# Kernel tuning notes

Hardware: AMD Instinct MI355X
Metric: run time of the kernel (lower is better)

The kernel has to match this reference:

```python
import jax, jax.numpy as jnp
import numpy as np

EPS = 1e-5      # BatchNorm eps (eval mode, running stats at init: mean=0, var=1)
SLOPE = 0.2     # LeakyReLU negative slope


def _knn_idx(x, k):
    # x: (B, N, D) -> (B, N, k) indices of k nearest neighbors (squared L2, feature space)
    sq = jnp.sum(x * x, axis=-1)                              # (B, N)
    dist = sq[:, :, None] + sq[:, None, :] - 2.0 * jnp.einsum('bnd,bmd->bnm', x, x)
    return jax.lax.top_k(-dist, k)[1]                         # nearest = largest of -dist


def _bn_lrelu(y, gamma, beta):
    # eval BatchNorm with running_mean=0, running_var=1, then LeakyReLU(0.2)
    y = y * (gamma / jnp.sqrt(1.0 + EPS)) + beta
    return jnp.where(y >= 0, y, SLOPE * y)


def _edge_conv(x, W, gamma, beta, k):
    # x: (B, N, D); W: (C_out, 2D). Returns (B, N, C_out) after max over k neighbors.
    idx = _knn_idx(x, k)                                      # (B, N, k)
    nb = jax.vmap(lambda xt, i: xt[i])(x, idx)                # (B, N, k, D) neighbor gather
    ctr = jnp.broadcast_to(x[:, :, None, :], nb.shape)
    feat = jnp.concatenate([nb - ctr, ctr], axis=-1)          # (B, N, k, 2D)
    y = jnp.einsum('bnkd,od->bnko', feat, W)                  # 1x1 conv (no bias)
    y = _bn_lrelu(y, gamma, beta)
    return jnp.max(y, axis=2)                                 # max-pool over neighbors


def setup_inputs() -> dict:
    key = jax.random.key(0)
    ks = jax.random.split(key, 16)
    B, N, k, out_dim = 8, 4096, 20, 512
    x = jax.random.normal(ks[0], (B, 3, N), dtype=jnp.float32)
    dims = [(64, 6), (64, 128), (128, 128), (256, 256), (out_dim, 512)]
    inp = {'x': x, 'k': k}
    for i, (co, ci) in enumerate(dims, start=1):
        inp[f'W{i}'] = jax.random.normal(ks[3 * i - 2], (co, ci), dtype=jnp.float32) * (1.0 / np.sqrt(ci))
        inp[f'g{i}'] = jax.random.uniform(ks[3 * i - 1], (co,), dtype=jnp.float32, minval=0.5, maxval=1.5)
        inp[f'b{i}'] = 0.1 * jax.random.normal(ks[3 * i], (co,), dtype=jnp.float32)
    return inp


def reference(x, W1, g1, b1, W2, g2, b2, W3, g3, b3, W4, g4, b4, W5, g5, b5, k):
    xt = jnp.transpose(x, (0, 2, 1))                          # (B, N, 3)
    x1 = _edge_conv(xt, W1, g1, b1, k)                        # (B, N, 64)
    x2 = _edge_conv(x1, W2, g2, b2, k)                        # (B, N, 64)
    x3 = _edge_conv(x2, W3, g3, b3, k)                        # (B, N, 128)
    x4 = _edge_conv(x3, W4, g4, b4, k)                        # (B, N, 256)
    h = jnp.concatenate([x1, x2, x3, x4], axis=-1)            # (B, N, 512)
    y = _bn_lrelu(jnp.einsum('bnd,od->bno', h, W5), g5, b5)   # (B, N, out_dim)
    return jnp.concatenate([jnp.max(y, axis=1), jnp.mean(y, axis=1)], axis=-1)  # (B, 2*out_dim)
```

## Files before the change

kernel.cpp:

```cpp
#include <hip/hip_runtime.h>
#include <math.h>

#define BATCH 8
#define N_PTS 4096
#define KNN 20
#define EPS_BN 1e-5f
#define SLOPE 0.2f
#define M_ROWS (BATCH * N_PTS)

typedef __attribute__((ext_vector_type(8))) short short8;
typedef __attribute__((ext_vector_type(4))) float float4v;
typedef __attribute__((ext_vector_type(16))) float float16v;

__device__ __forceinline__ unsigned short f2bf(float f) {
    unsigned u = __float_as_uint(f);
    unsigned r = (u + 0x7FFFu + ((u >> 16) & 1u)) >> 16;
    return (unsigned short)r;
}
__device__ __forceinline__ float bf2f(unsigned short h) {
    return __uint_as_float((unsigned)h << 16);
}

__global__ void convert_x1(const float* __restrict__ x,
                           unsigned short* __restrict__ xh, unsigned short* __restrict__ xl,
                           float* __restrict__ sq) {
    int i = blockIdx.x * blockDim.x + threadIdx.x;
    if (i >= M_ROWS) return;
    int b = i / N_PTS, n = i % N_PTS;
    float v[3], s = 0.f;
    #pragma unroll
    for (int d = 0; d < 3; ++d) {
        v[d] = x[((size_t)b * 3 + d) * N_PTS + n];
        s += v[d] * v[d];
    }
    sq[i] = s;
    #pragma unroll
    for (int d = 0; d < 32; ++d) {
        float f = (d < 3) ? v[d] : 0.f;
        unsigned short h = f2bf(f);
        xh[(size_t)i * 32 + d] = h;
        xl[(size_t)i * 32 + d] = f2bf(f - bf2f(h));
    }
}

__global__ void sqnorm_hl(const unsigned short* __restrict__ hh,
                          const unsigned short* __restrict__ hl,
                          int D, float* __restrict__ sq) {
    int w = threadIdx.x >> 6, lane = threadIdx.x & 63;
    int row = blockIdx.x * 4 + w;
    if (row >= M_ROWS) return;
    const unsigned short* ph = hh + (size_t)row * 512;
    const unsigned short* pl = hl + (size_t)row * 512;
    float s = 0.f;
    for (int d = lane; d < D; d += 64) {
        float v = bf2f(ph[d]) + bf2f(pl[d]);
        s += v * v;
    }
    #pragma unroll
    for (int off = 32; off > 0; off >>= 1) s += __shfl_down(s, off, 64);
    if (lane == 0) sq[row] = s;
}

__global__ void repack_edge_split(const float* __restrict__ W, int Co, int D, int KP,
                                  unsigned short* __restrict__ Wh, unsigned short* __restrict__ Wl) {
    int i = blockIdx.x * blockDim.x + threadIdx.x;
    int tot = 2 * Co * KP;
    if (i >= tot) return;
    int r = i / KP, d = i % KP;
    float v = 0.f;
    if (d < D) v = (r < Co) ? W[(size_t)r * 2 * D + d] : W[(size_t)(r - Co) * 2 * D + D + d];
    unsigned short h = f2bf(v);
    Wh[i] = h; Wl[i] = f2bf(v - bf2f(h));
}

__global__ void repack_w5_split(const float* __restrict__ W,
                                unsigned short* __restrict__ Wh, unsigned short* __restrict__ Wl) {
    int i = blockIdx.x * blockDim.x + threadIdx.x;
    if (i >= 512 * 512) return;
    float v = W[i];
    unsigned short h = f2bf(v);
    Wh[i] = h; Wl[i] = f2bf(v - bf2f(h));
}

template<int DPAD>
__global__ void
__launch_bounds__(256)
__attribute__((amdgpu_waves_per_eu(2, 2)))
knn_mfma(const unsigned short* __restrict__ Xh,
         const unsigned short* __restrict__ Xl,
         int strideX,
         const float* __restrict__ sq, int* __restrict__ idxout) {
    constexpr int KS = DPAD / 16;
    constexpr size_t MAIN  = (size_t)4096 * 4 + (size_t)256 * 17 * 4;
    constexpr size_t MERGE = (size_t)64 * 4 * KNN * 8;
    constexpr size_t POOL  = MAIN > MERGE ? MAIN : MERGE;
    __shared__ __align__(16) char smem[POOL];
    float* sqs = (float*)smem;
    float* scr = sqs + 4096;
    float*    kb = (float*)smem;
    unsigned* ib = (unsigned*)(kb + 64 * 4 * KNN);

    const int b = blockIdx.y;
    const int row0 = blockIdx.x * 64;
    const int tid = threadIdx.x;
    const int w = tid >> 6, lane = tid & 63;
    const int l31 = lane & 31, lh = lane >> 5;
    const int qg = w & 1, cg = w >> 1;

    const unsigned short* Xhb = Xh + (size_t)b * N_PTS * strideX;
    const unsigned short* Xlb = Xl + (size_t)b * N_PTS * strideX;
    const float* sqb = sq + (size_t)b * N_PTS;

    {
        const float4v* s4 = (const float4v*)sqb;
        float4v* d4 = (float4v*)sqs;
        #pragma unroll
        for (int it = 0; it < 4; ++it) d4[tid + it * 256] = s4[tid + it * 256];
    }
    __syncthreads();

    short8 qh[KS], ql[KS];
    {
        size_t qo = (size_t)(row0 + qg * 32 + l31) * strideX + lh * 8;
        #pragma unroll
        for (int ks = 0; ks < KS; ++ks) {
            qh[ks] = *(const short8*)(Xhb + qo + ks * 16);
            ql[ks] = *(const short8*)(Xlb + qo + ks * 16);
        }
    }

    float fv[KNN]; int fi[KNN];
    #pragma unroll
    for (int p = 0; p < KNN; ++p) { fv[p] = INFINITY; fi[p] = 0x7FFFFFFF; }

    const int scrb = tid * 17;

    #pragma unroll 1
    for (int c0 = 0; c0 < N_PTS; c0 += 64) {
        const int cbase = c0 + cg * 32;
        short8 ch[KS], cl[KS];
        size_t ro = (size_t)(cbase + l31) * strideX + lh * 8;
        #pragma unroll
        for (int ks = 0; ks < KS; ++ks) {
            ch[ks] = *(const short8*)(Xhb + ro + ks * 16);
            cl[ks] = *(const short8*)(Xlb + ro + ks * 16);
        }

        float16v acc = {};
        #pragma unroll
        for (int ks = 0; ks < KS; ++ks) {
            acc = __builtin_amdgcn_mfma_f32_32x32x16_bf16(ch[ks], qh[ks], acc, 0, 0, 0);
            acc = __builtin_amdgcn_mfma_f32_32x32x16_bf16(cl[ks], qh[ks], acc, 0, 0, 0);
            acc = __builtin_amdgcn_mfma_f32_32x32x16_bf16(ch[ks], ql[ks], acc, 0, 0, 0);
        }

        unsigned mask = 0;
        #pragma unroll
        for (int reg = 0; reg < 16; ++reg) {
            int crow = (reg & 3) + 8 * (reg >> 2) + 4 * lh;
            float v = fmaf(-2.f, acc[reg], sqs[cbase + crow]);
            scr[scrb + reg] = v;
            if (v < fv[KNN - 1]) mask |= (1u << reg);
        }
        while (mask) {
            int jj = __ffs(mask) - 1;
            mask &= mask - 1;
            float v = scr[scrb + jj];
            if (v < fv[KNN - 1]) {
                fv[KNN - 1] = v;
                fi[KNN - 1] = cbase + (jj & 3) + 8 * (jj >> 2) + 4 * lh;
                #pragma unroll
                for (int p = KNN - 1; p > 0; --p) {
                    float va = fv[p - 1], vb = fv[p];
                    int   ia = fi[p - 1], ic = fi[p];
                    bool sw = vb < va;
                    fv[p - 1] = sw ? vb : va; fv[p] = sw ? va : vb;
                    fi[p - 1] = sw ? ic : ia; fi[p] = sw ? ia : ic;
                }
            }
        }
    }
    __syncthreads();

    {
        int qloc = qg * 32 + l31;
        int list = cg * 2 + lh;
        int base = (qloc * 4 + list) * KNN;
        #pragma unroll
        for (int p = 0; p < KNN; ++p) { kb[base + p] = fv[p]; ib[base + p] = (unsigned)fi[p]; }
    }
    __syncthreads();

    if (tid < 64) {
        int base = tid * 4 * KNN;
        #pragma unroll
        for (int p = 0; p < KNN; ++p) { fv[p] = kb[base + p]; fi[p] = (int)ib[base + p]; }
        #pragma unroll 1
        for (int qq = KNN; qq < 4 * KNN; ++qq) {
            float    v  = kb[base + qq];
            int      ii = (int)ib[base + qq];
            bool ins = (v < fv[KNN - 1]) || (v == fv[KNN - 1] && ii < fi[KNN - 1]);
            if (ins) {
                fv[KNN - 1] = v; fi[KNN - 1] = ii;
                #pragma unroll
                for (int p = KNN - 1; p > 0; --p) {
                    float va = fv[p - 1], vb = fv[p];
                    int   ia = fi[p - 1], ic = fi[p];
                    bool sw = (vb < va) || (vb == va && ic < ia);
                    fv[p - 1] = sw ? vb : va; fv[p] = sw ? va : vb;
                    fi[p - 1] = sw ? ic : ia; fi[p] = sw ? ia : ic;
                }
            }
        }
        int* op = idxout + ((size_t)(b * N_PTS + row0 + tid)) * KNN;
        #pragma unroll
        for (int p = 0; p < KNN; ++p) op[p] = fi[p];
    }
}

__launch_bounds__(256)
__global__ void fgemm(const unsigned short* __restrict__ Ah, const unsigned short* __restrict__ Al,
                      int strideA, int K,
                      const unsigned short* __restrict__ Wh, const unsigned short* __restrict__ Wl,
                      int C, float* __restrict__ out, int fuse_bn,
                      const float* __restrict__ g, const float* __restrict__ beta) {
    __shared__ unsigned short AhS[128 * 40];
    __shared__ unsigned short AlS[128 * 40];
    __shared__ unsigned short BhS[128 * 40];
    __shared__ unsigned short BlS[128 * 40];

    const int c0 = blockIdx.x * 128;
    const int m0 = blockIdx.y * 128;
    const int tid = threadIdx.x;
    const int w = tid >> 6, lane = tid & 63;
    const int n = lane & 15, q = lane >> 4;

    float4v acc[2][8];
    #pragma unroll
    for (int rt = 0; rt < 2; ++rt)
        #pragma unroll
        for (int ct = 0; ct < 8; ++ct) acc[rt][ct] = (float4v){0.f, 0.f, 0.f, 0.f};

    for (int kk = 0; kk < K; kk += 32) {
        __syncthreads();
        for (int tt = tid; tt < 512; tt += 256) {
            int rr = tt >> 2, c8 = tt & 3;
            size_t oa = (size_t)(m0 + rr) * strideA + kk + c8 * 8;
            *(short8*)&AhS[rr * 40 + c8 * 8] = *(const short8*)(Ah + oa);
            *(short8*)&AlS[rr * 40 + c8 * 8] = *(const short8*)(Al + oa);
            size_t ob = (size_t)(c0 + rr) * K + kk + c8 * 8;
            *(short8*)&BhS[rr * 40 + c8 * 8] = *(const short8*)(Wh + ob);
            *(short8*)&BlS[rr * 40 + c8 * 8] = *(const short8*)(Wl + ob);
        }
        __syncthreads();

        short8 af[2][2];
        #pragma unroll
        for (int rt = 0; rt < 2; ++rt) {
            af[rt][0] = *(const short8*)&AhS[(w * 32 + rt * 16 + n) * 40 + q * 8];
            af[rt][1] = *(const short8*)&AlS[(w * 32 + rt * 16 + n) * 40 + q * 8];
        }
        #pragma unroll
        for (int ct = 0; ct < 8; ++ct) {
            short8 bh = *(const short8*)&BhS[(ct * 16 + n) * 40 + q * 8];
            short8 bl = *(const short8*)&BlS[(ct * 16 + n) * 40 + q * 8];
            #pragma unroll
            for (int rt = 0; rt < 2; ++rt) {
                acc[rt][ct] = __builtin_amdgcn_mfma_f32_16x16x32_bf16(af[rt][0], bh, acc[rt][ct], 0, 0, 0);
                acc[rt][ct] = __builtin_amdgcn_mfma_f32_16x16x32_bf16(af[rt][1], bh, acc[rt][ct], 0, 0, 0);
                acc[rt][ct] = __builtin_amdgcn_mfma_f32_16x16x32_bf16(af[rt][0], bl, acc[rt][ct], 0, 0, 0);
            }
        }
    }

    #pragma unroll
    for (int rt = 0; rt < 2; ++rt)
        #pragma unroll
        for (int ct = 0; ct < 8; ++ct) {
            int c = c0 + ct * 16 + n;
            float sc = 1.f, bt = 0.f;
            if (fuse_bn) { sc = g[c] / sqrtf(1.f + EPS_BN); bt = beta[c]; }
            #pragma unroll
            for (int e = 0; e < 4; ++e) {
                int m = m0 + w * 32 + rt * 16 + q * 4 + e;
                float v = acc[rt][ct][e];
                if (fuse_bn) { v = v * sc + bt; v = (v >= 0.f) ? v : SLOPE * v; }
                out[(size_t)m * C + c] = v;
            }
        }
}

__global__ void pool_kernel(const float* __restrict__ zc2, int Co,
                            const int* __restrict__ idx,
                            const float* __restrict__ g, const float* __restrict__ beta,
                            unsigned short* __restrict__ hh, unsigned short* __restrict__ hl,
                            int hoff) {
    int n = blockIdx.x, b = blockIdx.y;
    int o = threadIdx.x;
    size_t bn = (size_t)b * N_PTS + n;
    const int* ip = idx + bn * KNN;
    float zn   = zc2[bn * (size_t)(2 * Co) + o];
    float base = zc2[bn * (size_t)(2 * Co) + Co + o] - zn;
    float m = -INFINITY;
    #pragma unroll
    for (int j = 0; j < KNN; ++j) {
        size_t rr = (size_t)b * N_PTS + ip[j];
        m = fmaxf(m, zc2[rr * (size_t)(2 * Co) + o]);
    }
    float y = m + base;
    float sc = g[o] / sqrtf(1.f + EPS_BN);
    y = y * sc + beta[o];
    y = (y >= 0.f) ? y : SLOPE * y;
    unsigned short h = f2bf(y);
    hh[bn * 512 + hoff + o] = h;
    hl[bn * 512 + hoff + o] = f2bf(y - bf2f(h));
}

__global__ void reduce_partial(const float* __restrict__ y5,
                               float* __restrict__ pmax, float* __restrict__ psum) {
    int chunk = blockIdx.x, b = blockIdx.y, c = threadIdx.x;
    float mx = -INFINITY, sm = 0.f;
    for (int qq = 0; qq < 128; ++qq) {
        int n = chunk * 128 + qq;
        float v = y5[((size_t)b * N_PTS + n) * 512 + c];
        mx = fmaxf(mx, v);
        sm += v;
    }
    pmax[((size_t)b * 32 + chunk) * 512 + c] = mx;
    psum[((size_t)b * 32 + chunk) * 512 + c] = sm;
}

__global__ void reduce_final(const float* __restrict__ pmax,
                             const float* __restrict__ psum,
                             float* __restrict__ out) {
    int i = blockIdx.x * blockDim.x + threadIdx.x;
    if (i >= BATCH * 512) return;
    int b = i / 512, c = i % 512;
    float mx = -INFINITY, sm = 0.f;
    for (int qq = 0; qq < 32; ++qq) {
        mx = fmaxf(mx, pmax[((size_t)b * 32 + qq) * 512 + c]);
        sm += psum[((size_t)b * 32 + qq) * 512 + c];
    }
    out[(size_t)b * 1024 + c] = mx;
    out[(size_t)b * 1024 + 512 + c] = sm * (1.f / 4096.f);
}

extern "C" void kernel_launch(void* const* d_in, const int* in_sizes, int n_in,
                              void* d_out, int out_size, void* d_ws, size_t ws_size,
                              hipStream_t stream) {
    const float* x = (const float*)d_in[0];
    const float* W[5], *gg[5], *bb[5];
    for (int i = 0; i < 5; ++i) {
        W[i]  = (const float*)d_in[2 + 3 * i];
        gg[i] = (const float*)d_in[3 + 3 * i];
        bb[i] = (const float*)d_in[4 + 3 * i];
    }
    float* outp = (float*)d_out;

    char* wsb = (char*)d_ws;
    size_t off = 0;
    unsigned short* x1h = (unsigned short*)(wsb + off); off += (size_t)M_ROWS * 32 * 2;
    unsigned short* x1l = (unsigned short*)(wsb + off); off += (size_t)M_ROWS * 32 * 2;
    float* sq = (float*)(wsb + off); off += (size_t)M_ROWS * 4;
    int*   idx = (int*)(wsb + off); off += (size_t)M_ROWS * KNN * 4;
    unsigned short* Wh = (unsigned short*)(wsb + off); off += (size_t)512 * 512 * 2;
    unsigned short* Wl = (unsigned short*)(wsb + off); off += (size_t)512 * 512 * 2;
    unsigned short* hh = (unsigned short*)(wsb + off); off += (size_t)M_ROWS * 512 * 2;
    unsigned short* hl = (unsigned short*)(wsb + off); off += (size_t)M_ROWS * 512 * 2;
    float* zc2 = (float*)(wsb + off); off += (size_t)M_ROWS * 512 * 4;
    float* pmx = (float*)(wsb + off); off += (size_t)BATCH * 32 * 512 * 4;
    float* psm = (float*)(wsb + off); off += (size_t)BATCH * 32 * 512 * 4;
    (void)ws_size; (void)in_sizes; (void)n_in; (void)out_size;

    convert_x1<<<(M_ROWS + 255) / 256, 256, 0, stream>>>(x, x1h, x1l, sq);

    struct L { int D, Co, KP, hoff; };
    const L layers[4] = { {3, 64, 32, 0}, {64, 64, 64, 64}, {64, 128, 64, 128}, {128, 256, 128, 256} };

    for (int li = 0; li < 4; ++li) {
        const L& ly = layers[li];
        const unsigned short* Ahp;
        const unsigned short* Alp;
        int strideA;
        if (li == 0) { Ahp = x1h; Alp = x1l; strideA = 32; }
        else {
            int po = layers[li - 1].hoff;
            Ahp = hh + po; Alp = hl + po; strideA = 512;
            sqnorm_hl<<<M_ROWS / 4, 256, 0, stream>>>(Ahp, Alp, ly.D, sq);
        }

        if (li == 0)
            knn_mfma<32><<<dim3(N_PTS / 64, BATCH), 256, 0, stream>>>(Ahp, Alp, strideA, sq, idx);
        else if (ly.D == 64)
            knn_mfma<64><<<dim3(N_PTS / 64, BATCH), 256, 0, stream>>>(Ahp, Alp, strideA, sq, idx);
        else
            knn_mfma<128><<<dim3(N_PTS / 64, BATCH), 256, 0, stream>>>(Ahp, Alp, strideA, sq, idx);

        repack_edge_split<<<(2 * ly.Co * ly.KP + 255) / 256, 256, 0, stream>>>(
            W[li], ly.Co, ly.D, ly.KP, Wh, Wl);
        fgemm<<<dim3((2 * ly.Co) / 128, M_ROWS / 128), 256, 0, stream>>>(
            Ahp, Alp, strideA, ly.KP, Wh, Wl, 2 * ly.Co, zc2, 0, nullptr, nullptr);
        pool_kernel<<<dim3(N_PTS, BATCH), ly.Co, 0, stream>>>(
            zc2, ly.Co, idx, gg[li], bb[li], hh, hl, ly.hoff);
    }

    repack_w5_split<<<(512 * 512 + 255) / 256, 256, 0, stream>>>(W[4], Wh, Wl);
    fgemm<<<dim3(4, M_ROWS / 128), 256, 0, stream>>>(
        hh, hl, 512, 512, Wh, Wl, 512, zc2, 1, gg[4], bb[4]);

    reduce_partial<<<dim3(32, BATCH), 512, 0, stream>>>(zc2, pmx, psm);
    reduce_final<<<(BATCH * 512 + 255) / 256, 256, 0, stream>>>(pmx, psm, outp);
}
```

Measured before the change: 1.495 ms.

## Split kNN into threshold pass and exact tie-broken selection pass

The kNN kernel now runs two passes over all candidates. The first keeps only a value-only sorted top-K, using fminf/fmaxf, to find the Kth-smallest distance threshold. The second recomputes the distances and inserts only candidates at or below that threshold into an index-tracking list with index tie-breaking. This gives up a second full MFMA distance computation to get cheaper insertions with fewer registers in the first pass, and it removes the waves_per_eu(2,2) occupancy hint.

```diff
diff --git a/kernel.cpp b/kernel.cpp
--- a/kernel.cpp
+++ b/kernel.cpp
@@ -85,7 +85,6 @@
 template<int DPAD>
 __global__ void
 __launch_bounds__(256)
-__attribute__((amdgpu_waves_per_eu(2, 2)))
 knn_mfma(const unsigned short* __restrict__ Xh,
          const unsigned short* __restrict__ Xl,
          int strideX,
@@ -129,11 +128,11 @@
         }
     }
 
-    float fv[KNN]; int fi[KNN];
-    #pragma unroll
-    for (int p = 0; p < KNN; ++p) { fv[p] = INFINITY; fi[p] = 0x7FFFFFFF; }
-
     const int scrb = tid * 17;
+
+    float fv[KNN];
+    #pragma unroll
+    for (int p = 0; p < KNN; ++p) fv[p] = INFINITY;
 
     #pragma unroll 1
     for (int c0 = 0; c0 < N_PTS; c0 += 64) {
@@ -145,7 +144,6 @@
             ch[ks] = *(const short8*)(Xhb + ro + ks * 16);
             cl[ks] = *(const short8*)(Xlb + ro + ks * 16);
         }
-
         float16v acc = {};
         #pragma unroll
         for (int ks = 0; ks < KS; ++ks) {
@@ -153,7 +151,6 @@
             acc = __builtin_amdgcn_mfma_f32_32x32x16_bf16(cl[ks], qh[ks], acc, 0, 0, 0);
             acc = __builtin_amdgcn_mfma_f32_32x32x16_bf16(ch[ks], ql[ks], acc, 0, 0, 0);
         }
-
         unsigned mask = 0;
         #pragma unroll
         for (int reg = 0; reg < 16; ++reg) {
@@ -168,14 +165,62 @@
             float v = scr[scrb + jj];
             if (v < fv[KNN - 1]) {
                 fv[KNN - 1] = v;
-                fi[KNN - 1] = cbase + (jj & 3) + 8 * (jj >> 2) + 4 * lh;
                 #pragma unroll
                 for (int p = KNN - 1; p > 0; --p) {
-                    float va = fv[p - 1], vb = fv[p];
-                    int   ia = fi[p - 1], ic = fi[p];
-                    bool sw = vb < va;
-                    fv[p - 1] = sw ? vb : va; fv[p] = sw ? va : vb;
-                    fi[p - 1] = sw ? ic : ia; fi[p] = sw ? ia : ic;
+                    float a = fv[p - 1], c = fv[p];
+                    fv[p - 1] = fminf(a, c);
+                    fv[p]     = fmaxf(a, c);
+                }
+            }
+        }
+    }
+    const float thr = fv[KNN - 1];
+
+    float gv[KNN]; int gi[KNN];
+    #pragma unroll
+    for (int p = 0; p < KNN; ++p) { gv[p] = INFINITY; gi[p] = 0x7FFFFFFF; }
+
+    #pragma unroll 1
+    for (int c0 = 0; c0 < N_PTS; c0 += 64) {
+        const int cbase = c0 + cg * 32;
+        short8 ch[KS], cl[KS];
+        size_t ro = (size_t)(cbase + l31) * strideX + lh * 8;
+        #pragma unroll
+        for (int ks = 0; ks < KS; ++ks) {
+            ch[ks] = *(const short8*)(Xhb + ro + ks * 16);
+            cl[ks] = *(const short8*)(Xlb + ro + ks * 16);
+        }
+        float16v acc = {};
+        #pragma unroll
+        for (int ks = 0; ks < KS; ++ks) {
+            acc = __builtin_amdgcn_mfma_f32_32x32x16_bf16(ch[ks], qh[ks], acc, 0, 0, 0);
+            acc = __builtin_amdgcn_mfma_f32_32x32x16_bf16(cl[ks], qh[ks], acc, 0, 0, 0);
+            acc = __builtin_amdgcn_mfma_f32_32x32x16_bf16(ch[ks], ql[ks], acc, 0, 0, 0);
+        }
+        unsigned mask = 0;
+        #pragma unroll
+        for (int reg = 0; reg < 16; ++reg) {
+            int crow = (reg & 3) + 8 * (reg >> 2) + 4 * lh;
+            float v = fmaf(-2.f, acc[reg], sqs[cbase + crow]);
+            scr[scrb + reg] = v;
+            if (v <= thr) mask |= (1u << reg);
+        }
+        while (mask) {
+            int jj = __ffs(mask) - 1;
+            mask &= mask - 1;
+            float v = scr[scrb + jj];
+            int idxv = cbase + (jj & 3) + 8 * (jj >> 2) + 4 * lh;
+            bool ins = (v < gv[KNN - 1]) ||
+                       (v == gv[KNN - 1] && idxv < gi[KNN - 1]);
+            if (ins) {
+                gv[KNN - 1] = v; gi[KNN - 1] = idxv;
+                #pragma unroll
+                for (int p = KNN - 1; p > 0; --p) {
+                    float va = gv[p - 1], vb = gv[p];
+                    int   ia = gi[p - 1], ic = gi[p];
+                    bool sw = (vb < va) || (vb == va && ic < ia);
+                    gv[p - 1] = sw ? vb : va; gv[p] = sw ? va : vb;
+                    gi[p - 1] = sw ? ic : ia; gi[p] = sw ? ia : ic;
                 }
             }
         }
@@ -187,34 +232,35 @@
         int list = cg * 2 + lh;
         int base = (qloc * 4 + list) * KNN;
         #pragma unroll
-        for (int p = 0; p < KNN; ++p) { kb[base + p] = fv[p]; ib[base + p] = (unsigned)fi[p]; }
+        for (int p = 0; p < KNN; ++p) { kb[base + p] = gv[p]; ib[base + p] = (unsigned)gi[p]; }
     }
     __syncthreads();
 
     if (tid < 64) {
+        float mv[KNN]; int mi[KNN];
         int base = tid * 4 * KNN;
         #pragma unroll
-        for (int p = 0; p < KNN; ++p) { fv[p] = kb[base + p]; fi[p] = (int)ib[base + p]; }
+        for (int p = 0; p < KNN; ++p) { mv[p] = kb[base + p]; mi[p] = (int)ib[base + p]; }
         #pragma unroll 1
         for (int qq = KNN; qq < 4 * KNN; ++qq) {
-            float    v  = kb[base + qq];
-            int      ii = (int)ib[base + qq];
-            bool ins = (v < fv[KNN - 1]) || (v == fv[KNN - 1] && ii < fi[KNN - 1]);
+            float v  = kb[base + qq];
+            int   ii = (int)ib[base + qq];
+            bool ins = (v < mv[KNN - 1]) || (v == mv[KNN - 1] && ii < mi[KNN - 1]);
             if (ins) {
-                fv[KNN - 1] = v; fi[KNN - 1] = ii;
+                mv[KNN - 1] = v; mi[KNN - 1] = ii;
                 #pragma unroll
                 for (int p = KNN - 1; p > 0; --p) {
-                    float va = fv[p - 1], vb = fv[p];
-                    int   ia = fi[p - 1], ic = fi[p];
+                    float va = mv[p - 1], vb = mv[p];
+                    int   ia = mi[p - 1], ic = mi[p];
                     bool sw = (vb < va) || (vb == va && ic < ia);
-                    fv[p - 1] = sw ? vb : va; fv[p] = sw ? va : vb;
-                    fi[p - 1] = sw ? ic : ia; fi[p] = sw ? ia : ic;
+                    mv[p - 1] = sw ? vb : va; mv[p] = sw ? va : vb;
+                    mi[p - 1] = sw ? ic : ia; mi[p] = sw ? ia : ic;
                 }
             }
         }
         int* op = idxout + ((size_t)(b * N_PTS + row0 + tid)) * KNN;
         #pragma unroll
-        for (int p = 0; p < KNN; ++p) op[p] = fi[p];
+        for (int p = 0; p < KNN; ++p) op[p] = mi[p];
     }
 }
 
```

New measurement: 2.041 ms. +36.5%, slower.
